# Performance work log

Hardware: AMD Instinct MI355X
Metric: run time of the kernel (lower is better)

The kernel has to match this reference:

```python
import jax, jax.numpy as jnp
import numpy as np

SAMPLING_RATE = 16000.0
SINE_AMP = 0.1
NOISE_STD = 0.003
HARMONIC_NUM = 8  # dim = 9


def setup_inputs() -> dict:
    key = jax.random.key(0)
    k1, k2, k3, k4, k5, k6 = jax.random.split(key, 6)
    B, T, D = 16, 65536, HARMONIC_NUM + 1
    f0 = jax.random.uniform(k1, (B, T, 1), dtype=jnp.float32) * 400.0
    voiced = (jax.random.uniform(k2, (B, T, 1)) > 0.2).astype(jnp.float32)
    f0 = f0 * voiced
    # random initial phase per (batch, harmonic); first harmonic gets phase 0
    rand_init = jax.random.uniform(k3, (B, D), dtype=jnp.float32)
    rand_init = rand_init.at[:, 0].set(0.0)
    noise = jax.random.normal(k4, (B, T, D), dtype=jnp.float32)
    W = jax.random.normal(k5, (1, D), dtype=jnp.float32) * (1.0 / np.sqrt(D))
    b = jax.random.normal(k6, (1,), dtype=jnp.float32) * 0.01
    return {"f0": f0, "rand_init": rand_init, "noise": noise, "W": W, "b": b}


def reference(f0, rand_init, noise, W, b):
    # f0: [B, T, 1]; rand_init: [B, 9]; noise: [B, T, 9]; W: [1, 9]; b: [1]
    harmonics = jnp.arange(1, HARMONIC_NUM + 2, dtype=f0.dtype)  # [9]
    fn = f0 * harmonics                                          # [B, T, 9]
    rad = (fn / SAMPLING_RATE) % 1.0
    rad = rad.at[:, 0, :].add(rand_init)
    # phase-unwrap correction: subtract 1 wherever cumulative phase wrapped
    tmp = jnp.cumsum(rad, axis=1) % 1.0                          # [B, T, 9]
    diff = tmp[:, 1:, :] - tmp[:, :-1, :]                        # [B, T-1, 9]
    shift = jnp.concatenate(
        [jnp.zeros_like(rad[:, :1, :]), jnp.where(diff < 0, -1.0, 0.0)], axis=1
    )
    sines = jnp.sin(jnp.cumsum(rad + shift, axis=1) * (2.0 * jnp.pi)) * SINE_AMP
    uv = (f0 > 0.0).astype(f0.dtype)                             # [B, T, 1]
    noise_amp = uv * NOISE_STD + (1.0 - uv) * (SINE_AMP / 3.0)
    sine_waves = sines * uv + noise_amp * noise                  # [B, T, 9]
    sine_merge = jnp.tanh(sine_waves @ W.T + b)                  # [B, T, 1]
    return sine_merge
```

## Files before the change

kernel.cpp:

```cpp
#include <hip/hip_runtime.h>
#include <math.h>

#define B_N    16
#define T_LEN  65536
#define D_N    9
#define CHUNK  256
#define NCH    (T_LEN / CHUNK)

#define RCP_SR (1.0f / 16000.0f)

#define AS1C(p) ((const __attribute__((address_space(1))) void*)(p))
#define AS3(p)  ((__attribute__((address_space(3))) void*)(p))

__global__ __launch_bounds__(256) void k_chunksum(const float* __restrict__ f0,
                                                  float* __restrict__ csum) {
    int tid  = threadIdx.x;
    int lane = tid & 63;
    int wid  = tid >> 6;
    int chunk = blockIdx.x * 4 + wid;
    int b = chunk >> 8;
    int c = chunk & 255;
    int t = c * CHUNK + lane * 4;
    size_t bt = (size_t)b * T_LEN + t;

    const float4 fv = *reinterpret_cast<const float4*>(f0 + bt);
    double s = (double)(fv.x * RCP_SR) + (double)(fv.y * RCP_SR)
             + (double)(fv.z * RCP_SR) + (double)(fv.w * RCP_SR);

    #pragma unroll
    for (int off = 32; off >= 1; off >>= 1)
        s += __shfl_down(s, off, 64);

    if (lane == 0) {
        double fr = s - floor(s);
        csum[(size_t)b * NCH + c] = (float)fr;
    }
}

__global__ __launch_bounds__(256, 4) void k_main(const float* __restrict__ f0,
                                                 const float* __restrict__ noise,
                                                 const float* __restrict__ W,
                                                 const float* __restrict__ bias,
                                                 const float* __restrict__ rinit,
                                                 const float* __restrict__ csum,
                                                 float* __restrict__ out) {
    __shared__ float4 ldsbuf[4 * 576];
    int tid  = threadIdx.x;
    int lane = tid & 63;
    int wid  = tid >> 6;
    int chunk = blockIdx.x * 4 + wid;
    int b = chunk >> 8;
    int c = chunk & 255;
    int t = c * CHUNK + lane * 4;
    size_t bt = (size_t)b * T_LEN + t;

    const float4 fv  = *reinterpret_cast<const float4*>(f0 + bt);
    const float4 cs4 = *reinterpret_cast<const float4*>(csum + (size_t)b * NCH + lane * 4);

    int bu = __builtin_amdgcn_readfirstlane(b);
    const float* ri = rinit + bu * D_N;
    float wreg[D_N], rireg[D_N];
    #pragma unroll
    for (int h = 0; h < D_N; ++h) { wreg[h] = W[h]; rireg[h] = ri[h]; }
    float bb = bias[0];

    __builtin_amdgcn_sched_barrier(0);

    float4* ldsw = ldsbuf + wid * 576;
    const float* nbase = noise + ((size_t)b * T_LEN + (size_t)c * CHUNK) * D_N;
    #pragma unroll
    for (int q = 0; q < 9; ++q) {
        const float* g = nbase + (size_t)(lane + 64 * q) * 4;
        __builtin_amdgcn_global_load_lds(AS1C(g), AS3(ldsw + q * 64), 16, 0, 0);
    }
    __builtin_amdgcn_sched_barrier(0);

    float f[4] = {fv.x, fv.y, fv.z, fv.w};
    float s[4];
    float run = 0.0f;
    #pragma unroll
    for (int j = 0; j < 4; ++j) {
        run += f[j] * RCP_SR;
        s[j] = run;
    }
    float incl = run;
    #pragma unroll
    for (int off = 1; off < 64; off <<= 1) {
        float n = __shfl_up(incl, off, 64);
        if (lane >= off) incl += n;
    }

    int e0 = lane * 4;
    float pre = (e0 + 0 < c ? cs4.x : 0.0f)
              + (e0 + 1 < c ? cs4.y : 0.0f)
              + (e0 + 2 < c ? cs4.z : 0.0f)
              + (e0 + 3 < c ? cs4.w : 0.0f);
    #pragma unroll
    for (int off = 32; off >= 1; off >>= 1)
        pre += __shfl_xor(pre, off, 64);

    float base = __builtin_amdgcn_fractf(pre) + (incl - run);

    float fr[4], uvf[4], na[4];
    #pragma unroll
    for (int j = 0; j < 4; ++j) {
        fr[j] = __builtin_amdgcn_fractf(base + s[j]);
        bool uv = f[j] > 0.0f;
        uvf[j] = uv ? 0.1f : 0.0f;
        na[j]  = uv ? 0.003f : (float)(0.1 / 3.0);
    }

    asm volatile("s_waitcnt vmcnt(0)" ::: "memory");

    float nz[36];
    #pragma unroll
    for (int q = 0; q < 9; ++q) {
        float4 v4 = ldsw[9 * lane + q];
        nz[4 * q + 0] = v4.x; nz[4 * q + 1] = v4.y;
        nz[4 * q + 2] = v4.z; nz[4 * q + 3] = v4.w;
    }

    float acc[4] = {0.f, 0.f, 0.f, 0.f};
    #pragma unroll
    for (int h = 0; h < D_N; ++h) {
        const float hf = (float)(h + 1);
        const float wh = wreg[h];
        const float rih = rireg[h];
        #pragma unroll
        for (int j = 0; j < 4; ++j) {
            float x  = fmaf(fr[j], hf, rih);
            float xf = __builtin_amdgcn_fractf(x);
            float sn = __builtin_amdgcn_sinf(xf);
            float sw = fmaf(na[j], nz[j * 9 + h], sn * uvf[j]);
            acc[j] = fmaf(sw, wh, acc[j]);
        }
    }

    float4 o;
    #pragma unroll
    for (int j = 0; j < 4; ++j) {
        float y = acc[j] + bb;
        float e = __expf(2.0f * y);
        float r = __builtin_amdgcn_rcpf(e + 1.0f);
        float th = 1.0f - 2.0f * r;
        (&o.x)[j] = th;
    }
    *reinterpret_cast<float4*>(out + bt) = o;
}

extern "C" void kernel_launch(void* const* d_in, const int* in_sizes, int n_in,
                              void* d_out, int out_size, void* d_ws, size_t ws_size,
                              hipStream_t stream) {
    const float* f0    = (const float*)d_in[0];
    const float* rinit = (const float*)d_in[1];
    const float* noise = (const float*)d_in[2];
    const float* W     = (const float*)d_in[3];
    const float* bias  = (const float*)d_in[4];
    float* out = (float*)d_out;

    float* csum = (float*)d_ws;

    k_chunksum<<<(B_N * NCH) / 4, 256, 0, stream>>>(f0, csum);
    k_main<<<(B_N * NCH) / 4, 256, 0, stream>>>(f0, noise, W, bias, rinit, csum, out);
}
```

Measured before the change: 17.91 us.

## Factor noise dot product and consume LDS noise incrementally with staged waits

Splits the per-sample merge into two dot products: sines·W, computed before the noise arrives, and noise·W, accumulated per staged LDS slice. Each slice is read after a decreasing vmcnt wait instead of one full wait. The per-sample uv and noise-amplitude scaling is factored out and applied once at the end. The goal is to overlap sine computation with the async noise loads, cut per-harmonic multiplies, and drop the 36-register noise array. It relies on the async LDS loads completing in issue order so the vmcnt counts line up.

```diff
diff --git a/kernel.cpp b/kernel.cpp
--- a/kernel.cpp
+++ b/kernel.cpp
@@ -36,6 +36,16 @@
         csum[(size_t)b * NCH + c] = (float)fr;
     }
 }
+
+#define WAITV(n) asm volatile("s_waitcnt vmcnt(" #n ")" ::: "memory")
+
+#define CONS(Q) do {                                                        \
+    float4 v4 = ldsw[9 * lane + (Q)];                                       \
+    dacc[(4*(Q)+0)/9] = fmaf(wreg[(4*(Q)+0)%9], v4.x, dacc[(4*(Q)+0)/9]);   \
+    dacc[(4*(Q)+1)/9] = fmaf(wreg[(4*(Q)+1)%9], v4.y, dacc[(4*(Q)+1)/9]);   \
+    dacc[(4*(Q)+2)/9] = fmaf(wreg[(4*(Q)+2)%9], v4.z, dacc[(4*(Q)+2)/9]);   \
+    dacc[(4*(Q)+3)/9] = fmaf(wreg[(4*(Q)+3)%9], v4.w, dacc[(4*(Q)+3)/9]);   \
+} while (0)
 
 __global__ __launch_bounds__(256, 4) void k_main(const float* __restrict__ f0,
                                                  const float* __restrict__ noise,
@@ -110,17 +120,7 @@
         na[j]  = uv ? 0.003f : (float)(0.1 / 3.0);
     }
 
-    asm volatile("s_waitcnt vmcnt(0)" ::: "memory");
-
-    float nz[36];
-    #pragma unroll
-    for (int q = 0; q < 9; ++q) {
-        float4 v4 = ldsw[9 * lane + q];
-        nz[4 * q + 0] = v4.x; nz[4 * q + 1] = v4.y;
-        nz[4 * q + 2] = v4.z; nz[4 * q + 3] = v4.w;
-    }
-
-    float acc[4] = {0.f, 0.f, 0.f, 0.f};
+    float B[4] = {0.f, 0.f, 0.f, 0.f};
     #pragma unroll
     for (int h = 0; h < D_N; ++h) {
         const float hf = (float)(h + 1);
@@ -131,15 +131,25 @@
             float x  = fmaf(fr[j], hf, rih);
             float xf = __builtin_amdgcn_fractf(x);
             float sn = __builtin_amdgcn_sinf(xf);
-            float sw = fmaf(na[j], nz[j * 9 + h], sn * uvf[j]);
-            acc[j] = fmaf(sw, wh, acc[j]);
+            B[j] = fmaf(sn, wh, B[j]);
         }
     }
+
+    float dacc[4] = {0.f, 0.f, 0.f, 0.f};
+    WAITV(8); CONS(0);
+    WAITV(7); CONS(1);
+    WAITV(6); CONS(2);
+    WAITV(5); CONS(3);
+    WAITV(4); CONS(4);
+    WAITV(3); CONS(5);
+    WAITV(2); CONS(6);
+    WAITV(1); CONS(7);
+    WAITV(0); CONS(8);
 
     float4 o;
     #pragma unroll
     for (int j = 0; j < 4; ++j) {
-        float y = acc[j] + bb;
+        float y = fmaf(na[j], dacc[j], fmaf(uvf[j], B[j], bb));
         float e = __expf(2.0f * y);
         float r = __builtin_amdgcn_rcpf(e + 1.0f);
         float th = 1.0f - 2.0f * r;
```

New measurement: 17.90 us. About the same (-0.1%).
